# Kernel optimization log

Hardware: AMD Instinct MI355X
Metric: run time of the kernel (lower is better)

The kernel has to match this reference:

```python
import jax, jax.numpy as jnp
import numpy as np

B, T, C = 512, 256, 192
HEAD = 64

def setup_inputs() -> dict:
    key = jax.random.key(0)
    ks = jax.random.split(key, 5)
    return {
        "x": jax.random.normal(ks[0], (B, T, C), dtype=jnp.float32),
        "Wk": jax.random.normal(ks[1], (C, HEAD), dtype=jnp.float32) * (C ** -0.5),
        "Wq": jax.random.normal(ks[2], (C, HEAD), dtype=jnp.float32) * (C ** -0.5),
        "Wv": jax.random.normal(ks[3], (C, HEAD), dtype=jnp.float32) * (C ** -0.5),
        "pos_table": jax.random.normal(ks[4], (T, C), dtype=jnp.float32),
    }

def reference(x, Wk, Wq, Wv, pos_table):
    Bx, Tx, Cx = x.shape
    scale = Cx ** -0.5  # note: scales by n_embed, not head_size (faithful to source)
    k = jnp.einsum('btc,ch->bth', x, Wk)
    q = jnp.einsum('btc,ch->bth', x, Wq)
    v = jnp.einsum('btc,ch->bth', x, Wv)
    pe = pos_table[:Tx]                       # [T, C]
    pos_k = pe @ Wk                           # [T, H]
    pos_q = pe @ Wq                           # [T, H]
    bias = pos_k @ pos_q.T                    # [T, T]
    wei = jnp.einsum('bqh,bkh->bqk', q, k) * scale + bias
    causal = jnp.tril(jnp.ones((Tx, Tx), dtype=bool))
    wei = jnp.where(causal, wei, -jnp.inf)
    wei = jax.nn.softmax(wei, axis=-1)
    # dropout is identity in inference mode
    out = jnp.einsum('bqk,bkh->bqh', wei, v)
    return out
```

## Files before the change

### kernel.cpp

```cpp
#include <hip/hip_runtime.h>
#include <hip/hip_bf16.h>

typedef unsigned short u16;
typedef unsigned int u32;
using bf16x8 = __attribute__((ext_vector_type(8))) short;
using f32x4  = __attribute__((ext_vector_type(4))) float;

#define BB 512
#define TT 256
#define CC 192
#define HH 64

__device__ __forceinline__ u16 f2bf(float f) {
    __hip_bfloat16 h = __float2bfloat16(f);
    u16 u; __builtin_memcpy(&u, &h, 2); return u;
}


__global__ void wprep_kernel(const float* __restrict__ Wq,
                             const float* __restrict__ Wk,
                             const float* __restrict__ Wv,
                             u16* __restrict__ W_sw) {
    int gid  = blockIdx.x * 256 + threadIdx.x;
    int fid  = gid >> 6, lane = gid & 63;
    int n3   = fid / 6,  ks   = fid % 6;
    int l15  = lane & 15, quad = lane >> 4;
    const float* W = (n3 < 4) ? Wq : (n3 < 8) ? Wk : Wv;
    const int h = (n3 & 3) * 16 + l15;
    u16* dst = W_sw + (size_t)gid * 8;
    #pragma unroll
    for (int u = 0; u < 8; ++u) {
        int c = ks * 32 + quad * 8 + u;
        dst[u] = f2bf(W[c * HH + h]);
    }
}

__global__ void pos_kernel(const float* __restrict__ Wk,
                           const float* __restrict__ Wq,
                           const float* __restrict__ pe,
                           float* __restrict__ poskT, float* __restrict__ posqT) {
    int t = blockIdx.x * 4 + (threadIdx.x >> 6);
    int h = threadIdx.x & 63;
    float ak = 0.f, aq = 0.f;
    for (int c = 0; c < CC; ++c) {
        float p = pe[t * CC + c];
        ak += p * Wk[c * HH + h];
        aq += p * Wq[c * HH + h];
    }
    poskT[h * TT + t] = ak;
    posqT[h * TT + t] = aq;
}

__global__ void bias_kernel(const float* __restrict__ poskT,
                            const float* __restrict__ posqT,
                            float4* __restrict__ bias_sw) {
    const int i = blockIdx.x >> 4, jt = blockIdx.x & 15;
    if (jt > i) return;
    const int lane = threadIdx.x;
    const int l15 = lane & 15, quad = lane >> 4;
    const int tq = i * 16 + quad * 4;
    const int jc = jt * 16 + l15;
    float s[4] = {0.f, 0.f, 0.f, 0.f};
    for (int h = 0; h < HH; ++h) {
        float pq = posqT[h * TT + jc];
        #pragma unroll
        for (int r = 0; r < 4; ++r)
            s[r] += poskT[h * TT + tq + r] * pq;
    }
    bias_sw[blockIdx.x * 64 + lane] = make_float4(s[0], s[1], s[2], s[3]);
}


#define XP 200
#define VP 264
#define PP 40
#define P_ELEMS 640
#define XBUF 12800
#define Q_OFF 25600
#define K_OFF 58368
#define V_OFF 91136
#define LDS_TOTAL 124928

__global__ __launch_bounds__(512, 1)
void fused_kernel(const float* __restrict__ x,
                  const u16* __restrict__ W_sw,
                  const float4* __restrict__ bias_sw,
                  float* __restrict__ out) {
    extern __shared__ __align__(16) char smem[];
    u16* Qlds = (u16*)(smem + Q_OFF);
    u16* Klds = (u16*)(smem + K_OFF);
    u16* Vt   = (u16*)(smem + V_OFF);

    const int tid  = threadIdx.x;
    const int w    = tid >> 6;
    const int w4   = w & 3;
    const int mh   = w >> 2;
    const int lane = tid & 63;
    const int l15  = lane & 15;
    const int quad = lane >> 4;
    const int b    = blockIdx.x;

    const bf16x8* Wv8 = (const bf16x8*)W_sw;
    bf16x8 Wf[18];
    #pragma unroll
    for (int mat = 0; mat < 3; ++mat)
        #pragma unroll
        for (int ks = 0; ks < 6; ++ks)
            Wf[mat * 6 + ks] = Wv8[(((mat * 4 + w4) * 6) + ks) * 64 + lane];
    #pragma unroll
    for (int j = 0; j < 18; ++j)
        asm volatile("" : "+v"(Wf[j]));

    const int hs    = w4 >> 1;
    const int quadp = (w4 * 2 + (l15 >> 3)) & 3;
    const int uu    = l15 & 7;

    {
        const float* xb = x + (size_t)b * TT * CC;
        float4 vv[3];
        #pragma unroll
        for (int it = 0; it < 3; ++it)
            vv[it] = *(const float4*)(xb + (it * 512 + tid) * 4);
        u16* xs = (u16*)smem;
        #pragma unroll
        for (int it = 0; it < 3; ++it) {
            const int flat = (it * 512 + tid) * 4;
            const int row = flat / CC, col = flat % CC;
            uint2 pk;
            pk.x = (u32)f2bf(vv[it].x) | ((u32)f2bf(vv[it].y) << 16);
            pk.y = (u32)f2bf(vv[it].z) | ((u32)f2bf(vv[it].w) << 16);
            *(uint2*)&xs[row * XP + col] = pk;
        }
    }
    __syncthreads();

    #pragma unroll 1
    for (int c8 = 0; c8 < 8; ++c8) {
        const int cur = c8 & 1;
        float4 vnext[3];
        if (c8 < 7) {
            const float* xb = x + ((size_t)b * TT + (c8 + 1) * 32) * CC;
            #pragma unroll
            for (int it = 0; it < 3; ++it)
                vnext[it] = *(const float4*)(xb + (it * 512 + tid) * 4);
        }
        const u16* xs = (const u16*)(smem + cur * XBUF);
        f32x4 acc[3];
        #pragma unroll
        for (int i = 0; i < 3; ++i) acc[i] = {0.f, 0.f, 0.f, 0.f};
        #pragma unroll
        for (int ks = 0; ks < 6; ++ks) {
            const bf16x8 a = *(const bf16x8*)&xs[(mh * 16 + l15) * XP + ks * 32 + quad * 8];
            #pragma unroll
            for (int mat = 0; mat < 3; ++mat)
                acc[mat] = __builtin_amdgcn_mfma_f32_16x16x32_bf16(
                    a, Wf[mat * 6 + ks], acc[mat], 0, 0, 0);
        }
        {
            const int i_loc = c8 * 2 + mh;
            const int base  = (i_loc * 2 + hs) * 512 + (quadp * 16 + quad * 4) * 8 + uu;
            #pragma unroll
            for (int r = 0; r < 4; ++r) {
                Qlds[base + r * 8] = f2bf(acc[0][r]);
                Klds[base + r * 8] = f2bf(acc[1][r]);
            }
            #pragma unroll
            for (int r = 0; r < 4; ++r)
                Vt[(w4 * 16 + l15) * VP + i_loc * 16 + quad * 4 + r]
                    = f2bf(acc[2][r]);
        }
        if (c8 < 7) {
            u16* xsn = (u16*)(smem + (1 - cur) * XBUF);
            #pragma unroll
            for (int it = 0; it < 3; ++it) {
                const int flat = (it * 512 + tid) * 4;
                const int row = flat / CC, col = flat % CC;
                uint2 pk;
                pk.x = (u32)f2bf(vnext[it].x) | ((u32)f2bf(vnext[it].y) << 16);
                pk.y = (u32)f2bf(vnext[it].z) | ((u32)f2bf(vnext[it].w) << 16);
                *(uint2*)&xsn[row * XP + col] = pk;
            }
        }
        __syncthreads();
    }

    u16* Pw = (u16*)smem + w * P_ELEMS;
    const float scale = 0.07216878364870322f;
    const f32x4 zero4 = {0.f, 0.f, 0.f, 0.f};
    const bf16x8* qv = (const bf16x8*)Qlds;
    const bf16x8* kv = (const bf16x8*)Klds;

    #pragma unroll 1
    for (int mt = 0; mt < 2; ++mt) {
        const int i  = mt ? 15 - w : w;
        const int t0 = 16 * i;
        const int J  = i + 1;
        const int Pq = (J + 1) >> 1;

        const bf16x8 qf0 = qv[(i * 2 + 0) * 64 + lane];
        const bf16x8 qf1 = qv[(i * 2 + 1) * 64 + lane];

        f32x4 o[4];
        float m4[4], l4[4];
        #pragma unroll
        for (int n = 0; n < 4; ++n) o[n] = zero4;
        #pragma unroll
        for (int r = 0; r < 4; ++r) { m4[r] = -1e30f; l4[r] = 0.f; }

        #pragma unroll
        for (int p = 0; p < 8; ++p) {
            if (p < Pq) {
                const int jt0 = 2 * p, jt1 = 2 * p + 1;
                f32x4 sa = zero4, sb;
                {
                    bf16x8 k0 = kv[(jt0 * 2 + 0) * 64 + lane];
                    bf16x8 k1 = kv[(jt0 * 2 + 1) * 64 + lane];
                    sa = __builtin_amdgcn_mfma_f32_16x16x32_bf16(qf0, k0, sa, 0, 0, 0);
                    sa = __builtin_amdgcn_mfma_f32_16x16x32_bf16(qf1, k1, sa, 0, 0, 0);
                    const float4 b4 = bias_sw[(i * 16 + jt0) * 64 + lane];
                    sa[0] = sa[0] * scale + b4.x;
                    sa[1] = sa[1] * scale + b4.y;
                    sa[2] = sa[2] * scale + b4.z;
                    sa[3] = sa[3] * scale + b4.w;
                    if (jt0 == i) {
                        #pragma unroll
                        for (int r = 0; r < 4; ++r)
                            if (l15 > quad * 4 + r) sa[r] = -1e30f;
                    }
                }
                if (jt1 < J) {
                    sb = zero4;
                    bf16x8 k0 = kv[(jt1 * 2 + 0) * 64 + lane];
                    bf16x8 k1 = kv[(jt1 * 2 + 1) * 64 + lane];
                    sb = __builtin_amdgcn_mfma_f32_16x16x32_bf16(qf0, k0, sb, 0, 0, 0);
                    sb = __builtin_amdgcn_mfma_f32_16x16x32_bf16(qf1, k1, sb, 0, 0, 0);
                    const float4 b4 = bias_sw[(i * 16 + jt1) * 64 + lane];
                    sb[0] = sb[0] * scale + b4.x;
                    sb[1] = sb[1] * scale + b4.y;
                    sb[2] = sb[2] * scale + b4.z;
                    sb[3] = sb[3] * scale + b4.w;
                    if (jt1 == i) {
                        #pragma unroll
                        for (int r = 0; r < 4; ++r)
                            if (l15 > quad * 4 + r) sb[r] = -1e30f;
                    }
                } else {
                    sb[0] = -1e30f; sb[1] = -1e30f; sb[2] = -1e30f; sb[3] = -1e30f;
                }
                float t4[4];
                #pragma unroll
                for (int r = 0; r < 4; ++r) t4[r] = fmaxf(sa[r], sb[r]);
                #pragma unroll
                for (int d = 1; d < 16; d <<= 1) {
                    #pragma unroll
                    for (int r = 0; r < 4; ++r) t4[r] = fmaxf(t4[r], __shfl_xor(t4[r], d, 64));
                }
                float al[4];
                #pragma unroll
                for (int r = 0; r < 4; ++r) {
                    float mn = fmaxf(m4[r], t4[r]);
                    al[r] = __expf(m4[r] - mn);
                    m4[r] = mn;
                    l4[r] *= al[r];
                }
                #pragma unroll
                for (int n = 0; n < 4; ++n)
                #pragma unroll
                for (int r = 0; r < 4; ++r) o[n][r] *= al[r];
                #pragma unroll
                for (int r = 0; r < 4; ++r) {
                    float e0 = __expf(sa[r] - m4[r]);
                    float e1 = __expf(sb[r] - m4[r]);
                    l4[r] += e0 + e1;
                    Pw[(quad * 4 + r) * PP + l15]      = f2bf(e0);
                    Pw[(quad * 4 + r) * PP + 16 + l15] = f2bf(e1);
                }
                bf16x8 pa = *(const bf16x8*)&Pw[l15 * PP + quad * 8];
                #pragma unroll
                for (int n = 0; n < 4; ++n) {
                    bf16x8 bv = *(const bf16x8*)&Vt[(n * 16 + l15) * VP + p * 32 + quad * 8];
                    o[n] = __builtin_amdgcn_mfma_f32_16x16x32_bf16(pa, bv, o[n], 0, 0, 0);
                }
            }
        }
        #pragma unroll
        for (int d = 1; d < 16; d <<= 1) {
            #pragma unroll
            for (int r = 0; r < 4; ++r) l4[r] += __shfl_xor(l4[r], d, 64);
        }
        float rl4[4];
        #pragma unroll
        for (int r = 0; r < 4; ++r) rl4[r] = 1.f / l4[r];
        float* ob = out + ((size_t)b * TT + t0) * HH;
        #pragma unroll
        for (int n = 0; n < 4; ++n)
        #pragma unroll
        for (int r = 0; r < 4; ++r)
            ob[(quad * 4 + r) * HH + n * 16 + l15] = o[n][r] * rl4[r];
    }
}

extern "C" void kernel_launch(void* const* d_in, const int* in_sizes, int n_in,
                              void* d_out, int out_size, void* d_ws, size_t ws_size,
                              hipStream_t stream) {
    const float* x  = (const float*)d_in[0];
    const float* Wk = (const float*)d_in[1];
    const float* Wq = (const float*)d_in[2];
    const float* Wv = (const float*)d_in[3];
    const float* pe = (const float*)d_in[4];
    float* out = (float*)d_out;

    float*  poskT  = (float*)d_ws;
    float*  posqT  = poskT + TT * HH;
    float4* biassw = (float4*)(posqT + TT * HH);
    u16*    W_sw   = (u16*)((float*)biassw + TT * TT);

    static bool attr_set = false;
    if (!attr_set) {
        hipFuncSetAttribute(reinterpret_cast<const void*>(fused_kernel),
                            hipFuncAttributeMaxDynamicSharedMemorySize, LDS_TOTAL);
        attr_set = true;
    }

    wprep_kernel<<<18, 256, 0, stream>>>(Wq, Wk, Wv, W_sw);
    pos_kernel<<<TT / 4, 256, 0, stream>>>(Wk, Wq, pe, poskT, posqT);
    bias_kernel<<<256, 64, 0, stream>>>(poskT, posqT, biassw);
    fused_kernel<<<BB, 512, LDS_TOTAL, stream>>>(x, W_sw, biassw, out);
}
```

Before: 201.1 us.

## Stage Wq/Wk fragments in LDS and single-buffer the x tile

Copies the pre-swizzled Wq and Wk weight fragments into shared memory and reads them per k-step during the projection, keeping only the Wv fragments in registers. This cuts register pressure from 18 bf16x8 weight fragments to 6. The x staging buffer goes from double to single buffered, which adds a second barrier per chunk. In exchange the kernel does extra LDS reads inside the projection loop and needs more shared memory.

```diff
diff --git a/kernel.cpp b/kernel.cpp
--- a/kernel.cpp
+++ b/kernel.cpp
@@ -75,11 +75,11 @@
 #define VP 264
 #define PP 40
 #define P_ELEMS 640
-#define XBUF 12800
-#define Q_OFF 25600
-#define K_OFF 58368
-#define V_OFF 91136
-#define LDS_TOTAL 124928
+#define WQK_OFF 12800
+#define Q_OFF   61952
+#define K_OFF   94720
+#define V_OFF   127488
+#define LDS_TOTAL 161280
 
 __global__ __launch_bounds__(512, 1)
 void fused_kernel(const float* __restrict__ x,
@@ -100,16 +100,22 @@
     const int quad = lane >> 4;
     const int b    = blockIdx.x;
 
+    {
+        const uint4* src = (const uint4*)W_sw;
+        uint4* dst = (uint4*)(smem + WQK_OFF);
+        #pragma unroll
+        for (int it = 0; it < 6; ++it)
+            dst[it * 512 + tid] = src[it * 512 + tid];
+    }
+
     const bf16x8* Wv8 = (const bf16x8*)W_sw;
-    bf16x8 Wf[18];
+    bf16x8 WfV[6];
     #pragma unroll
-    for (int mat = 0; mat < 3; ++mat)
-        #pragma unroll
-        for (int ks = 0; ks < 6; ++ks)
-            Wf[mat * 6 + ks] = Wv8[(((mat * 4 + w4) * 6) + ks) * 64 + lane];
+    for (int ks = 0; ks < 6; ++ks)
+        WfV[ks] = Wv8[(((8 + w4) * 6) + ks) * 64 + lane];
     #pragma unroll
-    for (int j = 0; j < 18; ++j)
-        asm volatile("" : "+v"(Wf[j]));
+    for (int j = 0; j < 6; ++j)
+        asm volatile("" : "+v"(WfV[j]));
 
     const int hs    = w4 >> 1;
     const int quadp = (w4 * 2 + (l15 >> 3)) & 3;
@@ -136,25 +142,26 @@
 
     #pragma unroll 1
     for (int c8 = 0; c8 < 8; ++c8) {
-        const int cur = c8 & 1;
+        const bool hn = (c8 < 7);
         float4 vnext[3];
-        if (c8 < 7) {
+        if (hn) {
             const float* xb = x + ((size_t)b * TT + (c8 + 1) * 32) * CC;
             #pragma unroll
             for (int it = 0; it < 3; ++it)
                 vnext[it] = *(const float4*)(xb + (it * 512 + tid) * 4);
         }
-        const u16* xs = (const u16*)(smem + cur * XBUF);
+        const u16* xs = (const u16*)smem;
         f32x4 acc[3];
         #pragma unroll
         for (int i = 0; i < 3; ++i) acc[i] = {0.f, 0.f, 0.f, 0.f};
         #pragma unroll
         for (int ks = 0; ks < 6; ++ks) {
-            const bf16x8 a = *(const bf16x8*)&xs[(mh * 16 + l15) * XP + ks * 32 + quad * 8];
-            #pragma unroll
-            for (int mat = 0; mat < 3; ++mat)
-                acc[mat] = __builtin_amdgcn_mfma_f32_16x16x32_bf16(
-                    a, Wf[mat * 6 + ks], acc[mat], 0, 0, 0);
+            const bf16x8 a  = *(const bf16x8*)&xs[(mh * 16 + l15) * XP + ks * 32 + quad * 8];
+            const bf16x8 wq = *(const bf16x8*)(smem + WQK_OFF + ((w4 * 6 + ks) * 64 + lane) * 16);
+            const bf16x8 wk = *(const bf16x8*)(smem + WQK_OFF + (((4 + w4) * 6 + ks) * 64 + lane) * 16);
+            acc[0] = __builtin_amdgcn_mfma_f32_16x16x32_bf16(a, wq, acc[0], 0, 0, 0);
+            acc[1] = __builtin_amdgcn_mfma_f32_16x16x32_bf16(a, wk, acc[1], 0, 0, 0);
+            acc[2] = __builtin_amdgcn_mfma_f32_16x16x32_bf16(a, WfV[ks], acc[2], 0, 0, 0);
         }
         {
             const int i_loc = c8 * 2 + mh;
@@ -169,8 +176,9 @@
                 Vt[(w4 * 16 + l15) * VP + i_loc * 16 + quad * 4 + r]
                     = f2bf(acc[2][r]);
         }
-        if (c8 < 7) {
-            u16* xsn = (u16*)(smem + (1 - cur) * XBUF);
+        __syncthreads();
+        if (hn) {
+            u16* xsn = (u16*)smem;
             #pragma unroll
             for (int it = 0; it < 3; ++it) {
                 const int flat = (it * 512 + tid) * 4;
@@ -180,8 +188,8 @@
                 pk.y = (u32)f2bf(vnext[it].z) | ((u32)f2bf(vnext[it].w) << 16);
                 *(uint2*)&xsn[row * XP + col] = pk;
             }
-        }
-        __syncthreads();
+            __syncthreads();
+        }
     }
 
     u16* Pw = (u16*)smem + w * P_ELEMS;
```

Result: no change. 201.0 us (-0.1%).
